# Optimization experiments

Hardware: AMD Instinct MI355X
Metric: run time of the kernel (lower is better)

The kernel has to match this reference:

```python
import jax, jax.numpy as jnp
import numpy as np

N_CAM, N_REF, N_HEADS, EMBD = 6, 4, 8, 256
OUT = 10
L = OUT * OUT            # seq_len = output_size^2
HS = EMBD // N_HEADS
BS = 2


def setup_inputs() -> dict:
    key = jax.random.key(0)
    k1, k2, k3 = jax.random.split(key, 3)
    # C'*H'*W' must equal seq_len*embd = 100*256 = 25600 -> (256,10,10)
    single_frame_feature = jax.random.normal(k1, (BS, 1, N_CAM, 256, 10, 10), jnp.float32)
    bev_query = jax.random.normal(k2, (BS, L, EMBD), jnp.float32)
    W_v = jax.random.normal(k3, (N_CAM * EMBD, N_REF * EMBD), jnp.float32) / np.float32(np.sqrt(N_CAM * EMBD))
    b_v = jnp.zeros((N_REF * EMBD,), jnp.float32)
    return {"single_frame_feature": single_frame_feature, "bev_query": bev_query, "W_v": W_v, "b_v": b_v}


def reference(single_frame_feature, bev_query, W_v, b_v):
    bs, _, n_cam, C, H, W = single_frame_feature.shape
    _, seq_len, embd = bev_query.shape
    nh, hs, n_ref = N_HEADS, embd // N_HEADS, N_REF
    R = n_cam * n_ref  # repeat factor

    # (bs, n_cam, seq_len, embd) -- C*H*W == seq_len*embd by construction
    feat = single_frame_feature.reshape(bs, n_cam, seq_len, embd)

    # q: (bs, seq_len, nh, hs) repeated over cameras x ref points -> (bs, R*L, nh, hs)
    q = bev_query.reshape(bs, seq_len, nh, hs)
    q = jnp.tile(q, (1, R, 1, 1))

    # k: camera features broadcast over ref points, ordered (cam, ref, L)
    k = feat.reshape(bs, n_cam, 1, seq_len, nh, hs)
    k = jnp.broadcast_to(k, (bs, n_cam, n_ref, seq_len, nh, hs)).reshape(bs, R * seq_len, nh, hs)

    # v: per-location linear mixing cameras into n_ref value slots (self.v)
    v_in = feat.transpose(0, 2, 1, 3).reshape(bs, seq_len, n_cam * embd)
    v = v_in @ W_v + b_v                                   # (bs, L, n_ref*embd)
    v = v.reshape(bs, seq_len, n_ref, nh, hs).transpose(0, 2, 1, 3, 4)  # (bs, n_ref, L, nh, hs)
    v = jnp.broadcast_to(v[:, None], (bs, n_cam, n_ref, seq_len, nh, hs)).reshape(bs, R * seq_len, nh, hs)

    # scaled dot-product attention (dropout is identity at eval)
    scores = jnp.einsum('bqhd,bkhd->bhqk', q, k) / jnp.sqrt(jnp.float32(hs))
    att = jax.nn.softmax(scores, axis=-1)                  # (bs, nh, R*L, R*L)
    out = jnp.einsum('bhqk,bkhd->bqhd', att, v)            # (bs, R*L, nh, hs)

    # fold the R repeated views back to the BEV grid (uniform ref weights)
    out = out.reshape(bs, R, seq_len, embd).mean(axis=1)   # (bs, L, embd)
    return out
```

## Files before the change

### kernel.cpp

```cpp
#include <hip/hip_runtime.h>

#define N_CAM   6
#define N_HEADS 8
#define EMBD    256
#define HS      32
#define L       100
#define BS      2
#define CAM_STRIDE (L * EMBD)
#define CK      (N_CAM * L)

#define WS_WSUM 0
#define WS_KTR  (WS_WSUM + 1536 * 256)
#define WS_P    (WS_KTR + 2 * N_HEADS * 8 * CK * 4)
#define WS_E    (WS_P + 200 * 256 * 4)


__global__ __launch_bounds__(256) void prep_kernel(const float* __restrict__ feat,
                                                   const float4* __restrict__ Wv4,
                                                   float* __restrict__ ws) {
    const int t = threadIdx.x;
    if (blockIdx.x < 96) {
        __shared__ float tile[100 * 33];
        int blk = blockIdx.x;
        int b   = blk / 48;
        int rem = blk - b * 48;
        int cam = rem >> 3;
        int h   = rem & 7;
        const float4* src4 = reinterpret_cast<const float4*>(
            feat + (size_t)(b * N_CAM + cam) * CAM_STRIDE + h * HS);
        for (int idx = t; idx < 100 * 8; idx += 256) {
            int sk = idx >> 3;
            int d4 = idx & 7;
            float4 v = src4[sk * (EMBD / 4) + d4];
            float* dst = &tile[sk * 33 + d4 * 4];
            dst[0] = v.x; dst[1] = v.y; dst[2] = v.z; dst[3] = v.w;
        }
        __syncthreads();
        float4* ktr4 = reinterpret_cast<float4*>(ws + WS_KTR)
                     + (size_t)(b * N_HEADS + h) * 8 * CK + cam * L;
        for (int idx = t; idx < 8 * 100; idx += 256) {
            int d4 = idx / 100;
            int sk = idx - d4 * 100;
            const float* s = &tile[sk * 33 + d4 * 4];
            ktr4[(size_t)d4 * CK + sk] = make_float4(s[0], s[1], s[2], s[3]);
        }
    } else {
        int tid = (blockIdx.x - 96) * 256 + t;
        int i  = tid >> 6;
        int e4 = tid & 63;
        const float4* row = Wv4 + (size_t)i * 256;
        float4 a = row[e4];
        float4 b = row[64 + e4];
        float4 c = row[128 + e4];
        float4 d = row[192 + e4];
        float4 o;
        o.x = a.x + b.x + c.x + d.x;
        o.y = a.y + b.y + c.y + d.y;
        o.z = a.z + b.z + c.z + d.z;
        o.w = a.w + b.w + c.w + d.w;
        ((float4*)(ws + WS_WSUM))[(size_t)i * 64 + e4] = o;
    }
}

__global__ __launch_bounds__(256) void mid_kernel(const float* __restrict__ feat,
                                                  const float* __restrict__ query,
                                                  const float* __restrict__ ws_r,
                                                  float* __restrict__ ws_w) {
    const int t = threadIdx.x;
    if (blockIdx.x < 200) {
        __shared__ float  a_tile[4 * 384];
        __shared__ float4 red4[4 * 4 * 64];
        const int rg = blockIdx.x >> 2;
        const int c  = blockIdx.x & 3;
        const int r0 = rg * 4;
        const int k0 = c * 384;

        for (int i = t; i < 4 * 384; i += 256) {
            int j  = i / 384;
            int kk = i - j * 384;
            int k  = k0 + kk;
            int cam = k >> 8, e2 = k & 255;
            int row = r0 + j;
            int b = row >= 100;
            int s = row - b * 100;
            a_tile[i] = feat[(size_t)(b * N_CAM + cam) * CAM_STRIDE + s * EMBD + e2];
        }
        __syncthreads();

        const int g  = t >> 6;
        const int e4 = t & 63;
        float4 acc0 = {0.f,0.f,0.f,0.f}, acc1 = acc0, acc2 = acc0, acc3 = acc0;
        const float4* wp4 = (const float4*)(ws_r + WS_WSUM)
                          + (size_t)(k0 + g) * 64 + e4;
#pragma unroll 16
        for (int kk2 = 0; kk2 < 96; ++kk2) {
            float4 w = wp4[(size_t)kk2 * 256];
            int kk = kk2 * 4 + g;
            float a0 = a_tile[kk];
            float a1 = a_tile[384 + kk];
            float a2 = a_tile[768 + kk];
            float a3 = a_tile[1152 + kk];
            acc0.x += a0 * w.x; acc0.y += a0 * w.y; acc0.z += a0 * w.z; acc0.w += a0 * w.w;
            acc1.x += a1 * w.x; acc1.y += a1 * w.y; acc1.z += a1 * w.z; acc1.w += a1 * w.w;
            acc2.x += a2 * w.x; acc2.y += a2 * w.y; acc2.z += a2 * w.z; acc2.w += a2 * w.w;
            acc3.x += a3 * w.x; acc3.y += a3 * w.y; acc3.z += a3 * w.z; acc3.w += a3 * w.w;
        }

        red4[(g * 4 + 0) * 64 + e4] = acc0;
        red4[(g * 4 + 1) * 64 + e4] = acc1;
        red4[(g * 4 + 2) * 64 + e4] = acc2;
        red4[(g * 4 + 3) * 64 + e4] = acc3;
        __syncthreads();

        const int row = t >> 6, ee = t & 63;
        float4 s0 = red4[(0 * 4 + row) * 64 + ee];
        float4 s1 = red4[(1 * 4 + row) * 64 + ee];
        float4 s2 = red4[(2 * 4 + row) * 64 + ee];
        float4 s3 = red4[(3 * 4 + row) * 64 + ee];
        float4 s;
        s.x = s0.x + s1.x + s2.x + s3.x;
        s.y = s0.y + s1.y + s2.y + s3.y;
        s.z = s0.z + s1.z + s2.z + s3.z;
        s.w = s0.w + s1.w + s2.w + s3.w;

        float* P = ws_w + WS_P;
        size_t base = ((size_t)(r0 + row) * 256 + ee * 4) * 4 + c;
        P[base + 0 * 4] = s.x;
        P[base + 1 * 4] = s.y;
        P[base + 2 * 4] = s.z;
        P[base + 3 * 4] = s.w;
    } else {
        __shared__ float q_s[4 * 32];
        __shared__ float es[4 * CK];
        int idx = blockIdx.x - 200;
        int b   = idx / 200;
        int rem = idx - b * 200;
        int h   = rem / 25;
        int sqt = rem - h * 25;
        int sq0 = sqt * 4;

        if (t < 128)
            q_s[t] = query[(size_t)(b * L + sq0 + (t >> 5)) * EMBD + h * HS + (t & 31)];
        __syncthreads();

        const float scale = 0.17677669529663687f;
        const float4* kt4 = reinterpret_cast<const float4*>(ws_r + WS_KTR)
                          + (size_t)(b * N_HEADS + h) * 8 * CK;

#pragma unroll
        for (int i = 0; i < 3; ++i) {
            int ck = t + i * 256;
            if (ck < CK) {
                float acc0 = 0.f, acc1 = 0.f, acc2 = 0.f, acc3 = 0.f;
#pragma unroll
                for (int d4 = 0; d4 < 8; ++d4) {
                    float4 kv = kt4[(size_t)d4 * CK + ck];
                    const float* q0 = &q_s[0 * 32 + d4 * 4];
                    const float* q1 = &q_s[1 * 32 + d4 * 4];
                    const float* q2 = &q_s[2 * 32 + d4 * 4];
                    const float* q3 = &q_s[3 * 32 + d4 * 4];
                    acc0 += q0[0] * kv.x + q0[1] * kv.y + q0[2] * kv.z + q0[3] * kv.w;
                    acc1 += q1[0] * kv.x + q1[1] * kv.y + q1[2] * kv.z + q1[3] * kv.w;
                    acc2 += q2[0] * kv.x + q2[1] * kv.y + q2[2] * kv.z + q2[3] * kv.w;
                    acc3 += q3[0] * kv.x + q3[1] * kv.y + q3[2] * kv.z + q3[3] * kv.w;
                }
                es[0 * CK + ck] = __expf(acc0 * scale);
                es[1 * CK + ck] = __expf(acc1 * scale);
                es[2 * CK + ck] = __expf(acc2 * scale);
                es[3 * CK + ck] = __expf(acc3 * scale);
            }
        }
        __syncthreads();

        float* E = ws_w + WS_E;
        for (int p = t; p < 4 * L; p += 256) {
            int sj = p / 100, sk = p - sj * 100;
            float e = 0.f;
#pragma unroll
            for (int cam = 0; cam < N_CAM; ++cam)
                e += es[sj * CK + cam * L + sk];
            E[((size_t)(b * L + sq0 + sj) * N_HEADS + h) * L + sk] = e;
        }
    }
}

__global__ __launch_bounds__(256) void out_kernel(const float* __restrict__ ws,
                                                  const float* __restrict__ b_v,
                                                  float* __restrict__ out) {
    __shared__ float E_s[2 * N_HEADS * L];
    const int t   = threadIdx.x;
    const int b   = blockIdx.x / 50;
    const int sq0 = (blockIdx.x - b * 50) * 2;

    const float* E = ws + WS_E + (size_t)(b * L + sq0) * N_HEADS * L;
    for (int i = t; i < 2 * N_HEADS * L; i += 256) E_s[i] = E[i];
    __syncthreads();

    const int h = t >> 5;
    float sumE0 = 0.f, sumE1 = 0.f;
#pragma unroll 4
    for (int sk = 0; sk < L; ++sk) {
        sumE0 += E_s[h * L + sk];
        sumE1 += E_s[N_HEADS * L + h * L + sk];
    }

    float bias = b_v[t] + b_v[256 + t] + b_v[512 + t] + b_v[768 + t];

    const float4* p4 = (const float4*)(ws + WS_P) + (size_t)b * L * 256 + t;
    float acc0 = 0.f, acc1 = 0.f;
#pragma unroll 16
    for (int sk = 0; sk < L; ++sk) {
        float4 p = p4[(size_t)sk * 256];
        float s = p.x + p.y + p.z + p.w;
        acc0 += E_s[h * L + sk] * s;
        acc1 += E_s[N_HEADS * L + h * L + sk] * s;
    }

    out[(size_t)(b * L + sq0 + 0) * EMBD + t] = (acc0 + sumE0 * bias) * (0.25f / sumE0);
    out[(size_t)(b * L + sq0 + 1) * EMBD + t] = (acc1 + sumE1 * bias) * (0.25f / sumE1);
}

extern "C" void kernel_launch(void* const* d_in, const int* in_sizes, int n_in,
                              void* d_out, int out_size, void* d_ws, size_t ws_size,
                              hipStream_t stream) {
    const float* feat  = (const float*)d_in[0];
    const float* query = (const float*)d_in[1];
    const float4* Wv   = (const float4*)d_in[2];
    const float* bv    = (const float*)d_in[3];
    float* outp = (float*)d_out;
    float* ws   = (float*)d_ws;

    prep_kernel<<<480, 256, 0, stream>>>(feat, Wv, ws);
    mid_kernel<<<600, 256, 0, stream>>>(feat, query, ws, ws);
    out_kernel<<<100, 256, 0, stream>>>(ws, bv, outp);
}
```

Measured before the change: 94.38 us.

## Drop K transpose pre-pass and double rows per block in value GEMM

Removes the prep stage that transposed camera features into a K-major workspace layout. The score computation now reads key vectors directly from the feature tensor with strided float4 loads. The value-projection part of mid_kernel now handles 8 rows per block instead of 4, halving the number of GEMM blocks and reusing each weight load across more rows. Shared memory is unified into one aliased buffer. In exchange, key reads are less coalesced, there are more accumulator registers per thread, and fewer blocks are available for parallelism.

```diff
diff --git a/kernel.cpp b/kernel.cpp
--- a/kernel.cpp
+++ b/kernel.cpp
@@ -10,72 +10,43 @@
 #define CK      (N_CAM * L)
 
 #define WS_WSUM 0
-#define WS_KTR  (WS_WSUM + 1536 * 256)
-#define WS_P    (WS_KTR + 2 * N_HEADS * 8 * CK * 4)
+#define WS_P    (WS_WSUM + 1536 * 256)
 #define WS_E    (WS_P + 200 * 256 * 4)
 
 
-__global__ __launch_bounds__(256) void prep_kernel(const float* __restrict__ feat,
-                                                   const float4* __restrict__ Wv4,
+__global__ __launch_bounds__(256) void prep_kernel(const float4* __restrict__ Wv4,
                                                    float* __restrict__ ws) {
-    const int t = threadIdx.x;
-    if (blockIdx.x < 96) {
-        __shared__ float tile[100 * 33];
-        int blk = blockIdx.x;
-        int b   = blk / 48;
-        int rem = blk - b * 48;
-        int cam = rem >> 3;
-        int h   = rem & 7;
-        const float4* src4 = reinterpret_cast<const float4*>(
-            feat + (size_t)(b * N_CAM + cam) * CAM_STRIDE + h * HS);
-        for (int idx = t; idx < 100 * 8; idx += 256) {
-            int sk = idx >> 3;
-            int d4 = idx & 7;
-            float4 v = src4[sk * (EMBD / 4) + d4];
-            float* dst = &tile[sk * 33 + d4 * 4];
-            dst[0] = v.x; dst[1] = v.y; dst[2] = v.z; dst[3] = v.w;
-        }
-        __syncthreads();
-        float4* ktr4 = reinterpret_cast<float4*>(ws + WS_KTR)
-                     + (size_t)(b * N_HEADS + h) * 8 * CK + cam * L;
-        for (int idx = t; idx < 8 * 100; idx += 256) {
-            int d4 = idx / 100;
-            int sk = idx - d4 * 100;
-            const float* s = &tile[sk * 33 + d4 * 4];
-            ktr4[(size_t)d4 * CK + sk] = make_float4(s[0], s[1], s[2], s[3]);
-        }
-    } else {
-        int tid = (blockIdx.x - 96) * 256 + t;
-        int i  = tid >> 6;
-        int e4 = tid & 63;
-        const float4* row = Wv4 + (size_t)i * 256;
-        float4 a = row[e4];
-        float4 b = row[64 + e4];
-        float4 c = row[128 + e4];
-        float4 d = row[192 + e4];
-        float4 o;
-        o.x = a.x + b.x + c.x + d.x;
-        o.y = a.y + b.y + c.y + d.y;
-        o.z = a.z + b.z + c.z + d.z;
-        o.w = a.w + b.w + c.w + d.w;
-        ((float4*)(ws + WS_WSUM))[(size_t)i * 64 + e4] = o;
-    }
+    int tid = blockIdx.x * 256 + threadIdx.x;
+    int i  = tid >> 6;
+    int e4 = tid & 63;
+    const float4* row = Wv4 + (size_t)i * 256;
+    float4 a = row[e4];
+    float4 b = row[64 + e4];
+    float4 c = row[128 + e4];
+    float4 d = row[192 + e4];
+    float4 o;
+    o.x = a.x + b.x + c.x + d.x;
+    o.y = a.y + b.y + c.y + d.y;
+    o.z = a.z + b.z + c.z + d.z;
+    o.w = a.w + b.w + c.w + d.w;
+    ((float4*)(ws + WS_WSUM))[(size_t)i * 64 + e4] = o;
 }
 
 __global__ __launch_bounds__(256) void mid_kernel(const float* __restrict__ feat,
                                                   const float* __restrict__ query,
                                                   const float* __restrict__ ws_r,
                                                   float* __restrict__ ws_w) {
+    __shared__ __align__(16) float4 smem4[2048];
     const int t = threadIdx.x;
-    if (blockIdx.x < 200) {
-        __shared__ float  a_tile[4 * 384];
-        __shared__ float4 red4[4 * 4 * 64];
+
+    if (blockIdx.x < 100) {
+        float* a_tile = (float*)smem4;
         const int rg = blockIdx.x >> 2;
         const int c  = blockIdx.x & 3;
-        const int r0 = rg * 4;
+        const int r0 = rg * 8;
         const int k0 = c * 384;
 
-        for (int i = t; i < 4 * 384; i += 256) {
+        for (int i = t; i < 8 * 384; i += 256) {
             int j  = i / 384;
             int kk = i - j * 384;
             int k  = k0 + kk;
@@ -89,50 +60,56 @@
 
         const int g  = t >> 6;
         const int e4 = t & 63;
-        float4 acc0 = {0.f,0.f,0.f,0.f}, acc1 = acc0, acc2 = acc0, acc3 = acc0;
+        float4 acc[8];
+#pragma unroll
+        for (int j = 0; j < 8; ++j) acc[j] = make_float4(0.f, 0.f, 0.f, 0.f);
+
         const float4* wp4 = (const float4*)(ws_r + WS_WSUM)
                           + (size_t)(k0 + g) * 64 + e4;
-#pragma unroll 16
+#pragma unroll 8
         for (int kk2 = 0; kk2 < 96; ++kk2) {
             float4 w = wp4[(size_t)kk2 * 256];
             int kk = kk2 * 4 + g;
-            float a0 = a_tile[kk];
-            float a1 = a_tile[384 + kk];
-            float a2 = a_tile[768 + kk];
-            float a3 = a_tile[1152 + kk];
-            acc0.x += a0 * w.x; acc0.y += a0 * w.y; acc0.z += a0 * w.z; acc0.w += a0 * w.w;
-            acc1.x += a1 * w.x; acc1.y += a1 * w.y; acc1.z += a1 * w.z; acc1.w += a1 * w.w;
-            acc2.x += a2 * w.x; acc2.y += a2 * w.y; acc2.z += a2 * w.z; acc2.w += a2 * w.w;
-            acc3.x += a3 * w.x; acc3.y += a3 * w.y; acc3.z += a3 * w.z; acc3.w += a3 * w.w;
-        }
-
-        red4[(g * 4 + 0) * 64 + e4] = acc0;
-        red4[(g * 4 + 1) * 64 + e4] = acc1;
-        red4[(g * 4 + 2) * 64 + e4] = acc2;
-        red4[(g * 4 + 3) * 64 + e4] = acc3;
-        __syncthreads();
-
-        const int row = t >> 6, ee = t & 63;
-        float4 s0 = red4[(0 * 4 + row) * 64 + ee];
-        float4 s1 = red4[(1 * 4 + row) * 64 + ee];
-        float4 s2 = red4[(2 * 4 + row) * 64 + ee];
-        float4 s3 = red4[(3 * 4 + row) * 64 + ee];
-        float4 s;
-        s.x = s0.x + s1.x + s2.x + s3.x;
-        s.y = s0.y + s1.y + s2.y + s3.y;
-        s.z = s0.z + s1.z + s2.z + s3.z;
-        s.w = s0.w + s1.w + s2.w + s3.w;
+#pragma unroll
+            for (int j = 0; j < 8; ++j) {
+                float a = a_tile[j * 384 + kk];
+                acc[j].x += a * w.x;
+                acc[j].y += a * w.y;
+                acc[j].z += a * w.z;
+                acc[j].w += a * w.w;
+            }
+        }
+        __syncthreads();
+
+        float4* red4 = smem4;
+#pragma unroll
+        for (int j = 0; j < 8; ++j)
+            red4[(g * 8 + j) * 64 + e4] = acc[j];
+        __syncthreads();
 
         float* P = ws_w + WS_P;
-        size_t base = ((size_t)(r0 + row) * 256 + ee * 4) * 4 + c;
-        P[base + 0 * 4] = s.x;
-        P[base + 1 * 4] = s.y;
-        P[base + 2 * 4] = s.z;
-        P[base + 3 * 4] = s.w;
+        for (int q = t; q < 512; q += 256) {
+            int row = q >> 6;
+            int ee  = q & 63;
+            float4 s0 = red4[(0 * 8 + row) * 64 + ee];
+            float4 s1 = red4[(1 * 8 + row) * 64 + ee];
+            float4 s2 = red4[(2 * 8 + row) * 64 + ee];
+            float4 s3 = red4[(3 * 8 + row) * 64 + ee];
+            float4 s;
+            s.x = s0.x + s1.x + s2.x + s3.x;
+            s.y = s0.y + s1.y + s2.y + s3.y;
+            s.z = s0.z + s1.z + s2.z + s3.z;
+            s.w = s0.w + s1.w + s2.w + s3.w;
+            size_t base = ((size_t)(r0 + row) * 256 + ee * 4) * 4 + c;
+            P[base + 0 * 4] = s.x;
+            P[base + 1 * 4] = s.y;
+            P[base + 2 * 4] = s.z;
+            P[base + 3 * 4] = s.w;
+        }
     } else {
-        __shared__ float q_s[4 * 32];
-        __shared__ float es[4 * CK];
-        int idx = blockIdx.x - 200;
+        float* q_s = (float*)smem4;
+        float* es  = (float*)smem4 + 128;
+        int idx = blockIdx.x - 100;
         int b   = idx / 200;
         int rem = idx - b * 200;
         int h   = rem / 25;
@@ -144,17 +121,20 @@
         __syncthreads();
 
         const float scale = 0.17677669529663687f;
-        const float4* kt4 = reinterpret_cast<const float4*>(ws_r + WS_KTR)
-                          + (size_t)(b * N_HEADS + h) * 8 * CK;
+        const float4* f4 = reinterpret_cast<const float4*>(feat);
 
 #pragma unroll
         for (int i = 0; i < 3; ++i) {
             int ck = t + i * 256;
             if (ck < CK) {
+                int cam = ck / 100;
+                int sk  = ck - cam * 100;
+                const float4* kp = f4 + (size_t)(b * N_CAM + cam) * (CAM_STRIDE / 4)
+                                 + sk * 64 + h * 8;
                 float acc0 = 0.f, acc1 = 0.f, acc2 = 0.f, acc3 = 0.f;
 #pragma unroll
                 for (int d4 = 0; d4 < 8; ++d4) {
-                    float4 kv = kt4[(size_t)d4 * CK + ck];
+                    float4 kv = kp[d4];
                     const float* q0 = &q_s[0 * 32 + d4 * 4];
                     const float* q1 = &q_s[1 * 32 + d4 * 4];
                     const float* q2 = &q_s[2 * 32 + d4 * 4];
@@ -230,7 +210,7 @@
     float* outp = (float*)d_out;
     float* ws   = (float*)d_ws;
 
-    prep_kernel<<<480, 256, 0, stream>>>(feat, Wv, ws);
-    mid_kernel<<<600, 256, 0, stream>>>(feat, query, ws, ws);
+    prep_kernel<<<384, 256, 0, stream>>>(Wv, ws);
+    mid_kernel<<<500, 256, 0, stream>>>(feat, query, ws, ws);
     out_kernel<<<100, 256, 0, stream>>>(ws, bv, outp);
 }
```

New measurement: 101.3 us. 7.3% more time.
